# Kernel tuning notes

Hardware: AMD Instinct MI355X
Metric: run time of the kernel (lower is better)

The kernel has to match this reference:

```python
import jax, jax.numpy as jnp
import numpy as np

B, S1, S2, H = 8, 2048, 2048, 1024

def setup_inputs() -> dict:
    key = jax.random.key(0)
    k1, k2, kw, kb = jax.random.split(key, 4)
    hidden1 = jax.random.normal(k1, (B, S1, H), dtype=jnp.float32)
    hidden2 = jax.random.normal(k2, (B, S2, H), dtype=jnp.float32)
    W = jax.random.normal(kw, (H, H), dtype=jnp.float32) * 0.001
    bias = jax.random.normal(kb, (1,), dtype=jnp.float32) * 0.02
    return {"hidden1": hidden1, "hidden2": hidden2, "W": W, "bias": bias}

def reference(hidden1, hidden2, W, bias):
    # weight[b, i, j] = (hidden1 @ W)[b, i, :] . hidden2[b, j, :] + bias
    weight = jnp.einsum('bih,hk,bjk->bij', hidden1, W, hidden2) + bias[0]  # (B, S1, S2)
    # softmax over s1 (dim=1), then transpose-bmm with hidden1 -> (B, S2, H)
    a1 = jax.nn.softmax(weight, axis=1)
    hidden_1 = jnp.einsum('bij,bih->bjh', a1, hidden1)
    # softmax over s2 (dim=2), bmm with hidden2 -> (B, S1, H)
    a2 = jax.nn.softmax(weight, axis=2)
    hidden_2 = jnp.einsum('bij,bjh->bih', a2, hidden2)
    return (hidden_1, hidden_2)
```

## Files before the change

### kernel.cpp

```cpp
#include <hip/hip_runtime.h>
#include <stdint.h>

#define B_  8
#define S1_ 2048
#define S2_ 2048
#define H_  1024

typedef __attribute__((ext_vector_type(8))) short bf16x8;
typedef __attribute__((ext_vector_type(4))) float f32x4;
typedef unsigned short u16;

__device__ __forceinline__ u16 f2bf(float f){
  union { float f; uint32_t v; } x; x.f = f;
  uint32_t r = x.v + 0x7fffu + ((x.v >> 16) & 1u);
  return (u16)(r >> 16);
}
__device__ __forceinline__ u16 f2h(float f){
  union { _Float16 h; u16 u; } c; c.h = (_Float16)f; return c.u;
}
__device__ __forceinline__ float h2f(u16 u){
  union { _Float16 h; u16 u; } c; c.u = u; return (float)c.h;
}
__device__ __forceinline__ uint32_t pk2bf(float lo, float hi){
  uint32_t r;
  asm("v_cvt_pk_bf16_f32 %0, %1, %2" : "=v"(r) : "v"(lo), "v"(hi));
  return r;
}
__device__ __forceinline__ void async16(void* lds, const void* g){
  __builtin_amdgcn_global_load_lds(
      (const __attribute__((address_space(1))) uint32_t*)g,
      (__attribute__((address_space(3))) uint32_t*)lds, 16, 0, 0);
}

__global__ __launch_bounds__(256) void k_cvt_bf16(const float* __restrict__ in,
                                                  u16* __restrict__ out, long n){
  long i = ((long)blockIdx.x * 256 + threadIdx.x) * 8;
  const long stride = (long)gridDim.x * 256 * 8;
  for (; i < n; i += stride){
    float4 a = *(const float4*)(in + i);
    float4 b = *(const float4*)(in + i + 4);
    union { bf16x8 v; uint32_t w[4]; } o;
    o.w[0] = pk2bf(a.x, a.y); o.w[1] = pk2bf(a.z, a.w);
    o.w[2] = pk2bf(b.x, b.y); o.w[3] = pk2bf(b.z, b.w);
    *(bf16x8*)(out + i) = o.v;
  }
}

__global__ __launch_bounds__(256) void k_tcvt(const float* __restrict__ in,
                                              u16* __restrict__ out, int R, int Cc){
  __shared__ u16 t[32][33];
  in  += (long)blockIdx.z * R * Cc;
  out += (long)blockIdx.z * R * Cc;
  const int x = threadIdx.x & 31, y0 = threadIdx.x >> 5;
  const int bx = blockIdx.x * 32, by = blockIdx.y * 32;
  for (int r = y0; r < 32; r += 8) t[r][x] = f2bf(in[(long)(by + r) * Cc + bx + x]);
  __syncthreads();
  for (int r = y0; r < 32; r += 8) out[(long)(bx + r) * R + by + x] = t[x][r];
}

__global__ __launch_bounds__(256) void k_cvtT2(const float* __restrict__ in,
                                               u16* __restrict__ out_n,
                                               u16* __restrict__ out_t, int R, int Cc){
  __shared__ u16 t[64][68];
  in    += (long)blockIdx.z * R * Cc;
  out_n += (long)blockIdx.z * R * Cc;
  out_t += (long)blockIdx.z * R * Cc;
  const int tid = threadIdx.x;
  const int r0 = tid >> 4;
  const int c4 = (tid & 15) * 4;
  const int bx = blockIdx.x * 64;
  const int by = blockIdx.y * 64;
#pragma unroll
  for (int it = 0; it < 4; ++it){
    const int r = it*16 + r0;
    float4 v = *(const float4*)(in + (long)(by + r)*Cc + bx + c4);
    u16 b0 = f2bf(v.x), b1 = f2bf(v.y), b2 = f2bf(v.z), b3 = f2bf(v.w);
    ushort4 o; o.x = b0; o.y = b1; o.z = b2; o.w = b3;
    *(ushort4*)(out_n + (long)(by + r)*Cc + bx + c4) = o;
    t[r][c4] = b0; t[r][c4+1] = b1; t[r][c4+2] = b2; t[r][c4+3] = b3;
  }
  __syncthreads();
#pragma unroll
  for (int it = 0; it < 4; ++it){
    const int c = it*16 + r0;
    ushort4 o;
    o.x = t[c4  ][c]; o.y = t[c4+1][c]; o.z = t[c4+2][c]; o.w = t[c4+3][c];
    *(ushort4*)(out_t + (long)(bx + c)*R + by + c4) = o;
  }
}

__global__ __launch_bounds__(256) void k_cvtT2m(
    const float* __restrict__ in1, u16* __restrict__ n1, u16* __restrict__ t1,
    const float* __restrict__ in2, u16* __restrict__ n2, u16* __restrict__ t2,
    int R, int Cc){
  __shared__ u16 t[64][68];
  const int zb = blockIdx.z & 7;
  const bool second = blockIdx.z >= 8;
  const float* in = (second ? in2 : in1) + (long)zb * R * Cc;
  u16* out_n = (second ? n2 : n1) + (long)zb * R * Cc;
  u16* out_t = (second ? t2 : t1) + (long)zb * R * Cc;
  const int tid = threadIdx.x;
  const int r0 = tid >> 4;
  const int c4 = (tid & 15) * 4;
  const int bx = blockIdx.x * 64;
  const int by = blockIdx.y * 64;
#pragma unroll
  for (int it = 0; it < 4; ++it){
    const int r = it*16 + r0;
    float4 v = *(const float4*)(in + (long)(by + r)*Cc + bx + c4);
    u16 b0 = f2bf(v.x), b1 = f2bf(v.y), b2 = f2bf(v.z), b3 = f2bf(v.w);
    ushort4 o; o.x = b0; o.y = b1; o.z = b2; o.w = b3;
    *(ushort4*)(out_n + (long)(by + r)*Cc + bx + c4) = o;
    t[r][c4] = b0; t[r][c4+1] = b1; t[r][c4+2] = b2; t[r][c4+3] = b3;
  }
  __syncthreads();
#pragma unroll
  for (int it = 0; it < 4; ++it){
    const int c = it*16 + r0;
    ushort4 o;
    o.x = t[c4  ][c]; o.y = t[c4+1][c]; o.z = t[c4+2][c]; o.w = t[c4+3][c];
    *(ushort4*)(out_t + (long)(bx + c)*R + by + c4) = o;
  }
}

template<int OM, bool STATS>
__global__ __launch_bounds__(512) void k_gemm256(
    const u16* __restrict__ A, const u16* __restrict__ Bm, void* __restrict__ Cv,
    int M, int N, int K, long sA, long sB, long sC,
    float* __restrict__ rpmax, float* __restrict__ rpsum,
    float* __restrict__ cpmax, float* __restrict__ cpsum)
{
  const int GX = gridDim.x, GY = gridDim.y;
  const long plane = (long)GX * GY;
  const long tot = plane * gridDim.z;
  const long lin = blockIdx.x + (long)GX * (blockIdx.y + (long)GY * blockIdx.z);
  const long chunk = tot >> 3;
  const long swz = (lin & 7) * chunk + (lin >> 3);
  const int bz = (int)(swz / plane);
  const int rr = (int)(swz % plane);
  const int by_ = rr / GX, bx_ = rr % GX;

  A += (long)bz * sA; Bm += (long)bz * sB;
  __shared__ u16 lds[4 * 16384];
  const int tid = threadIdx.x, lane = tid & 63, w = tid >> 6;
  const int wm = w >> 2, wn = w & 3;
  const int brow = bx_ * 256, bcol = by_ * 256;

  f32x4 acc[8][4];
#pragma unroll
  for (int m=0;m<8;++m)
#pragma unroll
    for (int n=0;n<4;++n) acc[m][n] = (f32x4){0.f,0.f,0.f,0.f};

  const int fr = lane & 15;
  const int g8s = ((lane >> 4) ^ ((lane >> 1) & 3)) * 8;

  const int cc0 = w*128 + lane;
  const int cc1 = w*128 + 64 + lane;
  const int sl0 = (cc0 & 3) ^ ((cc0 >> 3) & 3);
  const int sl1 = (cc1 & 3) ^ ((cc1 >> 3) & 3);
  const u16* gA0 = A  + (long)(brow + (cc0 >> 2)) * K + sl0*8;
  const u16* gA1 = A  + (long)(brow + (cc1 >> 2)) * K + sl1*8;
  const u16* gB0 = Bm + (long)(bcol + (cc0 >> 2)) * K + sl0*8;
  const u16* gB1 = Bm + (long)(bcol + (cc1 >> 2)) * K + sl1*8;
  const int ldA0 = (w*128)*8, ldA1 = (w*128 + 64)*8;

  auto stage = [&](int buf, int t){
    u16* base = lds + buf*16384;
    async16(base + ldA0,        gA0 + t*32);
    async16(base + ldA1,        gA1 + t*32);
    async16(base + 8192 + ldA0, gB0 + t*32);
    async16(base + 8192 + ldA1, gB1 + t*32);
  };
  auto ldfrag = [&](int buf, bf16x8* a, bf16x8* b){
    const u16* At = lds + buf*16384;
    const u16* Bt = At + 8192;
#pragma unroll
    for (int n=0;n<4;++n) b[n] = *(const bf16x8*)(Bt + (wn*64 + n*16 + fr)*32 + g8s);
#pragma unroll
    for (int m=0;m<8;++m) a[m] = *(const bf16x8*)(At + (wm*128 + m*16 + fr)*32 + g8s);
  };

  const int NT = K >> 5;
  stage(0,0); stage(1,1); stage(2,2);
  asm volatile("s_waitcnt vmcnt(4)" ::: "memory");
  __builtin_amdgcn_s_barrier();

  bf16x8 a0[8], b0[4], a1[8], b1[4];
  ldfrag(0, a0, b0);

  for (int t = 0; t < NT; t += 2){
    if (t + 3 < NT) stage((t+3)&3, t+3);
    ldfrag((t+1)&3, a1, b1);
    __builtin_amdgcn_sched_barrier(0);
    __builtin_amdgcn_s_setprio(1);
#pragma unroll
    for (int m=0;m<8;++m)
#pragma unroll
      for (int n=0;n<4;++n)
        acc[m][n] = __builtin_amdgcn_mfma_f32_16x16x32_bf16(a0[m], b0[n], acc[m][n], 0,0,0);
    __builtin_amdgcn_s_setprio(0);
    asm volatile("s_waitcnt vmcnt(4)" ::: "memory");
    __builtin_amdgcn_s_barrier();

    if (t + 4 < NT) stage((t+4)&3, t+4);
    if (t + 2 < NT) ldfrag((t+2)&3, a0, b0);
    __builtin_amdgcn_sched_barrier(0);
    __builtin_amdgcn_s_setprio(1);
#pragma unroll
    for (int m=0;m<8;++m)
#pragma unroll
      for (int n=0;n<4;++n)
        acc[m][n] = __builtin_amdgcn_mfma_f32_16x16x32_bf16(a1[m], b1[n], acc[m][n], 0,0,0);
    __builtin_amdgcn_s_setprio(0);
    if (t + 2 < NT){
      asm volatile("s_waitcnt vmcnt(4)" ::: "memory");
      __builtin_amdgcn_s_barrier();
    }
  }

  const int crow = brow + wm*128 + (lane >> 4) * 4;
  const int ccol = bcol + wn*64 + fr;
  if constexpr (OM == 2){
    float* C = (float*)Cv + (long)bz * sC;
#pragma unroll
    for (int m=0;m<8;++m)
#pragma unroll
      for (int n=0;n<4;++n){
        f32x4 v = acc[m][n];
        float* cp = C + (long)(crow + m*16) * N + ccol + n*16;
#pragma unroll
        for (int q=0;q<4;++q) cp[(long)q*N] = v[q];
      }
  } else {
    u16* C = (u16*)Cv + (long)bz * sC;
#pragma unroll
    for (int m=0;m<8;++m)
#pragma unroll
      for (int n=0;n<4;++n){
        f32x4 v = acc[m][n];
        u16* cp = C + (long)(crow + m*16) * N + ccol + n*16;
#pragma unroll
        for (int q=0;q<4;++q) cp[(long)q*N] = OM ? f2h(v[q]) : f2bf(v[q]);
      }
  }

  if constexpr (STATS){
    const int hi = lane >> 4;
#pragma unroll
    for (int m=0;m<8;++m){
      f32x4 mx = acc[m][0];
#pragma unroll
      for (int n=1;n<4;++n)
#pragma unroll
        for (int q=0;q<4;++q) mx[q] = fmaxf(mx[q], acc[m][n][q]);
#pragma unroll
      for (int off=1; off<16; off<<=1)
#pragma unroll
        for (int q=0;q<4;++q) mx[q] = fmaxf(mx[q], __shfl_xor(mx[q], off));
      f32x4 sm = (f32x4){0.f,0.f,0.f,0.f};
#pragma unroll
      for (int n=0;n<4;++n)
#pragma unroll
        for (int q=0;q<4;++q) sm[q] += __expf(acc[m][n][q] - mx[q]);
#pragma unroll
      for (int off=1; off<16; off<<=1)
#pragma unroll
        for (int q=0;q<4;++q) sm[q] += __shfl_xor(sm[q], off);
      if (fr == 0){
        const int nb = by_*4 + wn;
        const long rb = ((long)bz*32 + nb)*2048 + brow + wm*128 + m*16 + hi*4;
#pragma unroll
        for (int q=0;q<4;++q){ rpmax[rb+q] = mx[q]; rpsum[rb+q] = sm[q]; }
      }
    }
#pragma unroll
    for (int n=0;n<4;++n){
      float mx = acc[0][n][0];
#pragma unroll
      for (int m=0;m<8;++m)
#pragma unroll
        for (int q=0;q<4;++q) mx = fmaxf(mx, acc[m][n][q]);
      mx = fmaxf(mx, __shfl_xor(mx, 16));
      mx = fmaxf(mx, __shfl_xor(mx, 32));
      float sm = 0.f;
#pragma unroll
      for (int m=0;m<8;++m)
#pragma unroll
        for (int q=0;q<4;++q) sm += __expf(acc[m][n][q] - mx);
      sm += __shfl_xor(sm, 16);
      sm += __shfl_xor(sm, 32);
      if (hi == 0){
        const int mb = bx_*2 + wm;
        const long cb = ((long)bz*16 + mb)*2048 + bcol + wn*64 + n*16 + fr;
        cpmax[cb] = mx; cpsum[cb] = sm;
      }
    }
  }
}

__global__ __launch_bounds__(256) void k_combine(
    const float* __restrict__ rpmax, const float* __restrict__ rpsum,
    const float* __restrict__ cpmax, const float* __restrict__ cpsum,
    float* __restrict__ rmax, float* __restrict__ rinv,
    float* __restrict__ cmax, float* __restrict__ cinv)
{
  const long i = (long)blockIdx.x*256 + threadIdx.x;
  const int b = (int)(i >> 11), r = (int)(i & 2047);
  if (blockIdx.y == 0){
    const float* pm = rpmax + ((long)b*32)*2048 + r;
    const float* ps = rpsum + ((long)b*32)*2048 + r;
    float m = -3.4e38f;
#pragma unroll
    for (int k=0;k<32;++k) m = fmaxf(m, pm[(long)k*2048]);
    float s = 0.f;
#pragma unroll
    for (int k=0;k<32;++k) s += ps[(long)k*2048] * __expf(pm[(long)k*2048] - m);
    rmax[i] = m; rinv[i] = 1.f / s;
  } else {
    const float* pm = cpmax + ((long)b*16)*2048 + r;
    const float* ps = cpsum + ((long)b*16)*2048 + r;
    float m = -3.4e38f;
#pragma unroll
    for (int k=0;k<16;++k) m = fmaxf(m, pm[(long)k*2048]);
    float s = 0.f;
#pragma unroll
    for (int k=0;k<16;++k) s += ps[(long)k*2048] * __expf(pm[(long)k*2048] - m);
    cmax[i] = m; cinv[i] = 1.f / s;
  }
}

__global__ __launch_bounds__(256) void k_p1t2(u16* __restrict__ Wg, u16* __restrict__ P2,
                                              const float* __restrict__ cmax,
                                              const float* __restrict__ cinv,
                                              const float* __restrict__ rmax,
                                              const float* __restrict__ rinv){
  const int ti = blockIdx.x, tj = blockIdx.y;
  if (tj < ti) return;
  const int b = blockIdx.z;
  u16* S = Wg + (long)b * S1_ * S2_;
  u16* P2b = P2 ? P2 + (long)b * S1_ * S2_ : (u16*)nullptr;
  const int I0 = ti*64, J0 = tj*64;
  __shared__ u16 tA[64][68];
  __shared__ u16 tB[64][68];
  __shared__ float scm[128], sci[128];
  const int tid = threadIdx.x;
  if (tid < 64){ scm[tid] = cmax[b*S2_ + J0 + tid]; sci[tid] = cinv[b*S2_ + J0 + tid]; }
  else if (tid < 128){ scm[tid] = cmax[b*S2_ + I0 + tid - 64]; sci[tid] = cinv[b*S2_ + I0 + tid - 64]; }
  __syncthreads();

  const int r0 = tid >> 3;
  const int c8 = (tid & 7) * 8;
#pragma unroll
  for (int it = 0; it < 2; ++it){
    const int r = it*32 + r0;
    bf16x8 v = *(const bf16x8*)(S + (long)(I0 + r)*S2_ + J0 + c8);
    const float rm = rmax[b*S1_ + I0 + r], ri = rinv[b*S1_ + I0 + r];
    union { bf16x8 v; uint32_t w[4]; } p2o;
#pragma unroll
    for (int k=0;k<4;++k){
      float x0 = h2f((u16)v[2*k]), x1 = h2f((u16)v[2*k+1]);
      p2o.w[k] = pk2bf(__expf(x0 - rm)*ri, __expf(x1 - rm)*ri);
      tA[r][c8+2*k]   = f2bf(__expf(x0 - scm[c8+2*k])   * sci[c8+2*k]);
      tA[r][c8+2*k+1] = f2bf(__expf(x1 - scm[c8+2*k+1]) * sci[c8+2*k+1]);
    }
    if (P2b) *(bf16x8*)(P2b + (long)(I0 + r)*S2_ + J0 + c8) = p2o.v;
  }
  if (ti != tj){
#pragma unroll
    for (int it = 0; it < 2; ++it){
      const int r = it*32 + r0;
      bf16x8 v = *(const bf16x8*)(S + (long)(J0 + r)*S2_ + I0 + c8);
      const float rm = rmax[b*S1_ + J0 + r], ri = rinv[b*S1_ + J0 + r];
      union { bf16x8 v; uint32_t w[4]; } p2o;
#pragma unroll
      for (int k=0;k<4;++k){
        float x0 = h2f((u16)v[2*k]), x1 = h2f((u16)v[2*k+1]);
        p2o.w[k] = pk2bf(__expf(x0 - rm)*ri, __expf(x1 - rm)*ri);
        tB[r][c8+2*k]   = f2bf(__expf(x0 - scm[64+c8+2*k])   * sci[64+c8+2*k]);
        tB[r][c8+2*k+1] = f2bf(__expf(x1 - scm[64+c8+2*k+1]) * sci[64+c8+2*k+1]);
      }
      if (P2b) *(bf16x8*)(P2b + (long)(J0 + r)*S2_ + I0 + c8) = p2o.v;
    }
  }
  __syncthreads();
  const int rr = tid >> 4;
  const int c4 = (tid & 15) * 4;
#pragma unroll
  for (int it = 0; it < 4; ++it){
    const int c = it*16 + rr;
    ushort4 o;
    o.x = tA[c4  ][c]; o.y = tA[c4+1][c]; o.z = tA[c4+2][c]; o.w = tA[c4+3][c];
    *(ushort4*)(S + (long)(J0 + c)*S2_ + I0 + c4) = o;
  }
  if (ti != tj){
#pragma unroll
    for (int it = 0; it < 4; ++it){
      const int c = it*16 + rr;
      ushort4 o;
      o.x = tB[c4  ][c]; o.y = tB[c4+1][c]; o.z = tB[c4+2][c]; o.w = tB[c4+3][c];
      *(ushort4*)(S + (long)(I0 + c)*S2_ + J0 + c4) = o;
    }
  }
}

__global__ __launch_bounds__(256) void k_gemm_h2(
    const u16* __restrict__ Wg, const u16* __restrict__ Bt, float* __restrict__ C,
    const float* __restrict__ rmax, const float* __restrict__ rinv)
{
  const int b = blockIdx.z;
  const u16* A  = Wg + (long)b * S1_ * S2_;
  const u16* Bp = Bt + (long)b * H_ * S2_;
  float* Cp = C + (long)b * S1_ * H_;

  __shared__ u16 As[128*32];
  __shared__ u16 Bs[128*32];
  const int tid = threadIdx.x, lane = tid & 63, w = tid >> 6;
  const int wr = (w >> 1) * 64, wc = (w & 1) * 64;
  const int brow = blockIdx.x * 128, bcol = blockIdx.y * 128;
  f32x4 acc[4][4];
#pragma unroll
  for (int m=0;m<4;++m)
#pragma unroll
    for (int n=0;n<4;++n) acc[m][n] = (f32x4){0.f,0.f,0.f,0.f};

  const int arow = w*16 + (lane >> 2);
  const int scol = (lane & 3) * 8;
  const u16* gA0 = A + (long)(brow + arow) * S2_ + scol;
  const u16* gA1 = gA0 + (long)64 * S2_;
  const float rm0 = rmax[b*S1_ + brow + arow],      ri0 = rinv[b*S1_ + brow + arow];
  const float rm1 = rmax[b*S1_ + brow + arow + 64], ri1 = rinv[b*S1_ + brow + arow + 64];
  u16* wA0 = As + arow*32 + scol;
  u16* wA1 = As + (arow+64)*32 + scol;

  const u16* gb = Bp + (long)(bcol + arow) * S2_ + scol;
  u16* lB0 = Bs + (w*16)*32;  u16* lB1 = Bs + (64 + w*16)*32;

  const int koff = (lane >> 4) * 8;
  const int fr = lane & 15;

  for (int k0 = 0; k0 < S2_; k0 += 32){
    bf16x8 x0 = *(const bf16x8*)(gA0 + k0);
    bf16x8 x1 = *(const bf16x8*)(gA1 + k0);
    async16(lB0, gb);  async16(lB1, gb + (long)64*S2_);
    gb += 32;
    union { bf16x8 v; uint32_t w4[4]; } y0, y1;
#pragma unroll
    for (int k=0;k<4;++k){
      y0.w4[k] = pk2bf(__expf(h2f((u16)x0[2*k])   - rm0) * ri0,
                       __expf(h2f((u16)x0[2*k+1]) - rm0) * ri0);
      y1.w4[k] = pk2bf(__expf(h2f((u16)x1[2*k])   - rm1) * ri1,
                       __expf(h2f((u16)x1[2*k+1]) - rm1) * ri1);
    }
    *(bf16x8*)wA0 = y0.v;
    *(bf16x8*)wA1 = y1.v;
    __syncthreads();
    bf16x8 af[4], bf[4];
#pragma unroll
    for (int m=0;m<4;++m) af[m] = *(const bf16x8*)(As + (wr + m*16 + fr)*32 + koff);
#pragma unroll
    for (int n=0;n<4;++n) bf[n] = *(const bf16x8*)(Bs + (wc + n*16 + fr)*32 + koff);
#pragma unroll
    for (int m=0;m<4;++m)
#pragma unroll
      for (int n=0;n<4;++n)
        acc[m][n] = __builtin_amdgcn_mfma_f32_16x16x32_bf16(af[m], bf[n], acc[m][n], 0,0,0);
    __syncthreads();
  }
  const int crow = brow + wr + (lane >> 4) * 4;
  const int ccol = bcol + wc + fr;
#pragma unroll
  for (int m=0;m<4;++m)
#pragma unroll
    for (int n=0;n<4;++n){
      f32x4 v = acc[m][n];
      float* cp = Cp + (long)(crow + m*16) * H_ + ccol + n*16;
#pragma unroll
      for (int q=0;q<4;++q) cp[(long)q*H_] = v[q];
    }
}

extern "C" void kernel_launch(void* const* d_in, const int* in_sizes, int n_in,
                              void* d_out, int out_size, void* d_ws, size_t ws_size,
                              hipStream_t stream)
{
  const float* h1 = (const float*)d_in[0];
  const float* h2 = (const float*)d_in[1];
  const float* W  = (const float*)d_in[2];
  float* out0 = (float*)d_out;
  float* out1 = out0 + (size_t)B_ * S2_ * H_;

  const long NE = (long)B_ * S1_ * H_;
  const long NS = (long)B_ * S1_ * S2_;

  char* ws = (char*)d_ws;
  size_t off = 0;
  float* rmax = (float*)(ws + off); off += (size_t)B_*S1_*4;
  float* rinv = (float*)(ws + off); off += (size_t)B_*S1_*4;
  float* cmax = (float*)(ws + off); off += (size_t)B_*S2_*4;
  float* cinv = (float*)(ws + off); off += (size_t)B_*S2_*4;
  u16* Wg  = (u16*)(ws + off);
  u16* WTb = Wg;
  off += (size_t)NS*2;
  u16* h1t = (u16*)(ws + off); off += (size_t)NE*2;

  const bool use_p2 = ws_size >= off + (size_t)NS*2;
  u16* P2 = use_p2 ? (u16*)(ws + off) : (u16*)nullptr;
  size_t off2 = off + (use_p2 ? (size_t)NS*2 : 0);
  const bool ws_h2t = ws_size >= off2 + (size_t)NE*2;

  u16* h1b = (u16*)out0;
  u16* h2b = (u16*)out0 + NE;
  u16* h2t = ws_h2t ? (u16*)(ws + off2) : (u16*)out0;
  u16* Qb  = (u16*)out1;
  float* rpmax = (float*)((u16*)out1 + NE);
  float* rpsum = rpmax + (size_t)B_*32*2048;
  float* cpmax = rpsum + (size_t)B_*32*2048;
  float* cpsum = cpmax + (size_t)B_*16*2048;

  if (ws_h2t){
    k_cvtT2m<<<dim3(16,32,16), 256, 0, stream>>>(h1, h1b, h1t, h2, h2b, h2t, S1_, H_);
  } else {
    k_cvtT2<<<dim3(16,32,8), 256, 0, stream>>>(h1, h1b, h1t, S1_, H_);
    k_cvt_bf16<<<dim3(4096), 256, 0, stream>>>(h2, h2b, NE);
  }
  k_tcvt<<<dim3(32,32,1), 256, 0, stream>>>(W, WTb, H_, H_);
  k_gemm256<0,false><<<dim3(8, 4, 8), 512, 0, stream>>>(h1b, WTb, Qb, S1_, H_, H_,
        (long)S1_*H_, 0L, (long)S1_*H_, nullptr, nullptr, nullptr, nullptr);
  if (!ws_h2t){
    k_tcvt<<<dim3(32,64,8), 256, 0, stream>>>(h2, h2t, S2_, H_);
  }
  k_gemm256<1,true><<<dim3(8, 8, 8), 512, 0, stream>>>(Qb, h2b, Wg, S1_, S2_, H_,
        (long)S1_*H_, (long)S2_*H_, (long)S1_*S2_, rpmax, rpsum, cpmax, cpsum);
  k_combine<<<dim3(64, 2), 256, 0, stream>>>(rpmax, rpsum, cpmax, cpsum,
                                             rmax, rinv, cmax, cinv);
  if (use_p2){
    k_p1t2<<<dim3(32,32,8), 256, 0, stream>>>(Wg, P2, cmax, cinv, rmax, rinv);
    k_gemm256<2,false><<<dim3(8, 4, 8), 512, 0, stream>>>(P2, h2t, out1, S1_, H_, S2_,
          (long)S1_*S2_, (long)H_*S2_, (long)S1_*H_, nullptr, nullptr, nullptr, nullptr);
  } else {
    k_gemm_h2<<<dim3(16, 8, 8), 256, 0, stream>>>(Wg, h2t, out1, rmax, rinv);
    k_p1t2<<<dim3(32,32,8), 256, 0, stream>>>(Wg, (u16*)nullptr, cmax, cinv, rmax, rinv);
  }
  k_gemm256<2,false><<<dim3(8, 4, 8), 512, 0, stream>>>(Wg, h1t, out0, S2_, H_, S1_,
        (long)S1_*S2_, (long)H_*S1_, (long)S2_*H_, nullptr, nullptr, nullptr, nullptr);
}
```

Measured before the change: 357.4 us.

## Switch GEMM main loop to BK=64 double-buffered tiles with 8-way XOR swizzle

The 256x256 GEMM main loop drops the 4-stage BK=32 LDS pipeline. It now uses 2 LDS buffers of BK=64 tiles, with one global stage and one barrier per 64-wide K step, and a new 8-way XOR swizzle on the wider rows. Fragments are loaded just before each MFMA group instead of being software-prefetched into a second register set. This halves the barriers and waits per K, but exposes LDS read latency before each MFMA block and leaves only one tile of prefetch depth.

```diff
diff --git a/kernel.cpp b/kernel.cpp
--- a/kernel.cpp
+++ b/kernel.cpp
@@ -141,7 +141,7 @@
   const int by_ = rr / GX, bx_ = rr % GX;
 
   A += (long)bz * sA; Bm += (long)bz * sB;
-  __shared__ u16 lds[4 * 16384];
+  __shared__ u16 lds[2 * 32768];
   const int tid = threadIdx.x, lane = tid & 63, w = tid >> 6;
   const int wm = w >> 2, wn = w & 3;
   const int brow = bx_ * 256, bcol = by_ * 256;
@@ -153,73 +153,71 @@
     for (int n=0;n<4;++n) acc[m][n] = (f32x4){0.f,0.f,0.f,0.f};
 
   const int fr = lane & 15;
-  const int g8s = ((lane >> 4) ^ ((lane >> 1) & 3)) * 8;
-
-  const int cc0 = w*128 + lane;
-  const int cc1 = w*128 + 64 + lane;
-  const int sl0 = (cc0 & 3) ^ ((cc0 >> 3) & 3);
-  const int sl1 = (cc1 & 3) ^ ((cc1 >> 3) & 3);
-  const u16* gA0 = A  + (long)(brow + (cc0 >> 2)) * K + sl0*8;
-  const u16* gA1 = A  + (long)(brow + (cc1 >> 2)) * K + sl1*8;
-  const u16* gB0 = Bm + (long)(bcol + (cc0 >> 2)) * K + sl0*8;
-  const u16* gB1 = Bm + (long)(bcol + (cc1 >> 2)) * K + sl1*8;
-  const int ldA0 = (w*128)*8, ldA1 = (w*128 + 64)*8;
-
+  const int hi = lane >> 4;
+  const int sk0 = (((0*4)+hi) ^ (fr & 7)) * 8;
+  const int sk1 = (((1*4)+hi) ^ (fr & 7)) * 8;
+
+  const u16* gAs[4]; const u16* gBs[4];
+#pragma unroll
+  for (int j=0;j<4;++j){
+    const int cc = (w*4 + j)*64 + lane;
+    const int row = cc >> 3;
+    const int sl = (cc & 7) ^ (row & 7);
+    gAs[j] = A  + (long)(brow + row) * K + sl*8;
+    gBs[j] = Bm + (long)(bcol + row) * K + sl*8;
+  }
   auto stage = [&](int buf, int t){
-    u16* base = lds + buf*16384;
-    async16(base + ldA0,        gA0 + t*32);
-    async16(base + ldA1,        gA1 + t*32);
-    async16(base + 8192 + ldA0, gB0 + t*32);
-    async16(base + 8192 + ldA1, gB1 + t*32);
+    u16* base = lds + buf*32768;
+#pragma unroll
+    for (int j=0;j<4;++j) async16(base + (w*4+j)*512, gAs[j] + (long)t*64);
+#pragma unroll
+    for (int j=0;j<4;++j) async16(base + 16384 + (w*4+j)*512, gBs[j] + (long)t*64);
   };
-  auto ldfrag = [&](int buf, bf16x8* a, bf16x8* b){
-    const u16* At = lds + buf*16384;
-    const u16* Bt = At + 8192;
-#pragma unroll
-    for (int n=0;n<4;++n) b[n] = *(const bf16x8*)(Bt + (wn*64 + n*16 + fr)*32 + g8s);
-#pragma unroll
-    for (int m=0;m<8;++m) a[m] = *(const bf16x8*)(At + (wm*128 + m*16 + fr)*32 + g8s);
+  auto ldfragK = [&](int buf, int sk, bf16x8* a, bf16x8* b){
+    const u16* At = lds + buf*32768;
+    const u16* Bt = At + 16384;
+#pragma unroll
+    for (int n=0;n<4;++n) b[n] = *(const bf16x8*)(Bt + (wn*64 + n*16 + fr)*64 + sk);
+#pragma unroll
+    for (int m=0;m<8;++m) a[m] = *(const bf16x8*)(At + (wm*128 + m*16 + fr)*64 + sk);
   };
 
-  const int NT = K >> 5;
-  stage(0,0); stage(1,1); stage(2,2);
-  asm volatile("s_waitcnt vmcnt(4)" ::: "memory");
+  const int NT = K >> 6;
+  stage(0, 0);
+  asm volatile("s_waitcnt vmcnt(0)" ::: "memory");
   __builtin_amdgcn_s_barrier();
 
-  bf16x8 a0[8], b0[4], a1[8], b1[4];
-  ldfrag(0, a0, b0);
-
-  for (int t = 0; t < NT; t += 2){
-    if (t + 3 < NT) stage((t+3)&3, t+3);
-    ldfrag((t+1)&3, a1, b1);
-    __builtin_amdgcn_sched_barrier(0);
+  for (int t = 0; t < NT; ++t){
+    const int cur = t & 1;
+    if (t + 1 < NT) stage(cur ^ 1, t + 1);
+
+    bf16x8 a[8], b[4];
+    ldfragK(cur, sk0, a, b);
     __builtin_amdgcn_s_setprio(1);
 #pragma unroll
     for (int m=0;m<8;++m)
 #pragma unroll
       for (int n=0;n<4;++n)
-        acc[m][n] = __builtin_amdgcn_mfma_f32_16x16x32_bf16(a0[m], b0[n], acc[m][n], 0,0,0);
+        acc[m][n] = __builtin_amdgcn_mfma_f32_16x16x32_bf16(a[m], b[n], acc[m][n], 0,0,0);
     __builtin_amdgcn_s_setprio(0);
-    asm volatile("s_waitcnt vmcnt(4)" ::: "memory");
-    __builtin_amdgcn_s_barrier();
-
-    if (t + 4 < NT) stage((t+4)&3, t+4);
-    if (t + 2 < NT) ldfrag((t+2)&3, a0, b0);
-    __builtin_amdgcn_sched_barrier(0);
+
+    ldfragK(cur, sk1, a, b);
     __builtin_amdgcn_s_setprio(1);
 #pragma unroll
     for (int m=0;m<8;++m)
 #pragma unroll
       for (int n=0;n<4;++n)
-        acc[m][n] = __builtin_amdgcn_mfma_f32_16x16x32_bf16(a1[m], b1[n], acc[m][n], 0,0,0);
+        acc[m][n] = __builtin_amdgcn_mfma_f32_16x16x32_bf16(a[m], b[n], acc[m][n], 0,0,0);
     __builtin_amdgcn_s_setprio(0);
-    if (t + 2 < NT){
-      asm volatile("s_waitcnt vmcnt(4)" ::: "memory");
+
+    if (t + 1 < NT){
+      asm volatile("s_waitcnt vmcnt(0)" ::: "memory");
+      asm volatile("s_waitcnt lgkmcnt(0)" ::: "memory");
       __builtin_amdgcn_s_barrier();
     }
   }
 
-  const int crow = brow + wm*128 + (lane >> 4) * 4;
+  const int crow = brow + wm*128 + hi * 4;
   const int ccol = bcol + wn*64 + fr;
   if constexpr (OM == 2){
     float* C = (float*)Cv + (long)bz * sC;
@@ -246,7 +244,6 @@
   }
 
   if constexpr (STATS){
-    const int hi = lane >> 4;
 #pragma unroll
     for (int m=0;m<8;++m){
       f32x4 mx = acc[m][0];
```

New measurement: 355.2 us (median of 2 runs). Within noise of the previous version (-0.6%).
